# Kernel tuning notes

Hardware: AMD Instinct MI355X
Metric: run time of the kernel (lower is better)

The kernel has to match this reference:

```python
import jax, jax.numpy as jnp
import numpy as np
from jax import lax

DIM = 192
HEADS = 4
HIDDEN = int(DIM * 2.66)  # 510


def _conv1x1(x, w, b):
    # x: [B,C,H,W], w: [O,C], b: [O]
    return jnp.einsum('bchw,oc->bohw', x, w) + b[None, :, None, None]


def _dwconv3x3(x, w, b):
    # x: [B,C,H,W], w: [C,1,3,3], b: [C]
    c = x.shape[1]
    y = lax.conv_general_dilated(x, w, window_strides=(1, 1), padding='SAME',
                                 feature_group_count=c,
                                 dimension_numbers=('NCHW', 'OIHW', 'NCHW'))
    return y + b[None, :, None, None]


def _layernorm_c(x, w, b):
    # LayerNorm over channel dim (torch LayerNorm(dim) applied to b,(hw),c)
    mu = jnp.mean(x, axis=1, keepdims=True)
    var = jnp.mean((x - mu) ** 2, axis=1, keepdims=True)
    xn = (x - mu) / jnp.sqrt(var + 1e-5)
    return xn * w[None, :, None, None] + b[None, :, None, None]


def _l2norm(x):
    # F.normalize(dim=-1), eps=1e-12
    n = jnp.sqrt(jnp.sum(x * x, axis=-1, keepdims=True))
    return x / jnp.maximum(n, 1e-12)


def setup_inputs() -> dict:
    key = jax.random.key(0)
    ks = jax.random.split(key, 16)
    s = 0.02
    d, h2 = DIM, HIDDEN * 2
    return {
        'x': jax.random.normal(ks[0], (4, DIM, 128, 128), jnp.float32),
        'ln1_w': jnp.ones((d,), jnp.float32),
        'ln1_b': jnp.zeros((d,), jnp.float32),
        'qkv_w': jax.random.normal(ks[1], (3 * d, d), jnp.float32) * s,
        'qkv_b': jnp.zeros((3 * d,), jnp.float32),
        'qkv_dw_w': jax.random.normal(ks[2], (3 * d, 1, 3, 3), jnp.float32) * s,
        'qkv_dw_b': jnp.zeros((3 * d,), jnp.float32),
        'temperature': jnp.ones((HEADS, 1, 1), jnp.float32),
        'proj_w': jax.random.normal(ks[3], (d, d), jnp.float32) * s,
        'proj_b': jnp.zeros((d,), jnp.float32),
        'ln2_w': jnp.ones((d,), jnp.float32),
        'ln2_b': jnp.zeros((d,), jnp.float32),
        'pin_w': jax.random.normal(ks[4], (h2, d), jnp.float32) * s,
        'pin_b': jnp.zeros((h2,), jnp.float32),
        'dw_w': jax.random.normal(ks[5], (h2, 1, 3, 3), jnp.float32) * s,
        'dw_b': jnp.zeros((h2,), jnp.float32),
        'pout_w': jax.random.normal(ks[6], (d, HIDDEN), jnp.float32) * s,
        'pout_b': jnp.zeros((d,), jnp.float32),
    }


def _attention(x, qkv_w, qkv_b, qkv_dw_w, qkv_dw_b, temperature, proj_w, proj_b):
    b, c, h, w = x.shape
    qkv = _dwconv3x3(_conv1x1(x, qkv_w, qkv_b), qkv_dw_w, qkv_dw_b)
    q, k, v = jnp.split(qkv, 3, axis=1)
    ch = c // HEADS

    def heads(t):  # b (head c) h w -> b head c (h w)
        return t.reshape(b, HEADS, ch, h * w)

    q, k, v = heads(q), heads(k), heads(v)
    q = _l2norm(q)
    k = _l2norm(k)
    attn = jnp.einsum('bhcn,bhdn->bhcd', q, k) * temperature[None]  # [b,H,ch,ch]
    attn = jax.nn.softmax(attn, axis=-1)
    out = jnp.einsum('bhcd,bhdn->bhcn', attn, v)
    out = out.reshape(b, c, h, w)
    return _conv1x1(out, proj_w, proj_b)


def _ffn(x, pin_w, pin_b, dw_w, dw_b, pout_w, pout_b):
    y = _conv1x1(x, pin_w, pin_b)
    y = _dwconv3x3(y, dw_w, dw_b)
    x1, x2 = jnp.split(y, 2, axis=1)
    y = jax.nn.gelu(x1, approximate=False) * x2
    return _conv1x1(y, pout_w, pout_b)


def reference(x, ln1_w, ln1_b, qkv_w, qkv_b, qkv_dw_w, qkv_dw_b, temperature,
              proj_w, proj_b, ln2_w, ln2_b, pin_w, pin_b, dw_w, dw_b,
              pout_w, pout_b):
    x = x + _attention(_layernorm_c(x, ln1_w, ln1_b), qkv_w, qkv_b,
                       qkv_dw_w, qkv_dw_b, temperature, proj_w, proj_b)
    x = x + _ffn(_layernorm_c(x, ln2_w, ln2_b), pin_w, pin_b, dw_w, dw_b,
                 pout_w, pout_b)
    return x
```

## Files before the change

### kernel.cpp

```cpp
#include <hip/hip_runtime.h>
#include <math.h>

typedef long long i64;
typedef unsigned short u16;
typedef unsigned int u32;

#define HW 16384
#define DIM 192
#define NHEADS 4
#define CH 48
#define OQKV 576
#define HID 510
#define H2 1020
#define NB 4
#define NSPLIT 64
#define QKPAD 132

typedef __attribute__((ext_vector_type(8))) short short8v;
typedef __attribute__((ext_vector_type(4))) float float4v;

__device__ __forceinline__ u16 f2bf(float f) {
  union { float f; u32 u; } v; v.f = f;
  u32 r = v.u + 0x7FFF + ((v.u >> 16) & 1);
  return (u16)(r >> 16);
}
__device__ __forceinline__ float bflo(u32 w) {
  union { u32 u; float f; } v; v.u = w << 16; return v.f;
}
__device__ __forceinline__ float bfhi(u32 w) {
  union { u32 u; float f; } v; v.u = w & 0xFFFF0000u; return v.f;
}
__device__ __forceinline__ float bf1(u16 h) {
  union { u32 u; float f; } v; v.u = ((u32)h) << 16; return v.f;
}
__device__ __forceinline__ u32 pk(float a, float b) {
  return (u32)f2bf(a) | ((u32)f2bf(b) << 16);
}
__device__ __forceinline__ float gelu_f(float x) {
  float y = 0.7978845608f * (x + 0.044715f * x * x * x);
  float ay = fabsf(y);
  float e = __expf(-2.f * ay);
  float t = (1.f - e) / (1.f + e);
  t = (y < 0.f) ? -t : t;
  return 0.5f * x * (1.f + t);
}

#define GLL16(gp, lp) __builtin_amdgcn_global_load_lds( \
    (const __attribute__((address_space(1))) u32*)(gp), \
    (__attribute__((address_space(3))) u32*)(lp), 16, 0, 0)

__global__ __launch_bounds__(256) void ln_kernel(const float* __restrict__ x,
    const float* __restrict__ w, const float* __restrict__ b, u16* __restrict__ yT) {
  __shared__ float st[32][193];
  __shared__ float red[2][8][32];
  __shared__ float murs[2][32];
  const float* xb = x + (i64)blockIdx.y * DIM * HW;
  u16* yb = yT + (i64)blockIdx.y * (i64)HW * DIM;
  int tid = threadIdx.x;
  int g = tid >> 5, p = tid & 31;
  int pix0 = blockIdx.x * 32;
  float s = 0.f, ss = 0.f;
  #pragma unroll
  for (int i = 0; i < 24; ++i) {
    float t = xb[(i64)(g * 24 + i) * HW + pix0 + p];
    st[p][g * 24 + i] = t; s += t; ss += t * t;
  }
  red[0][g][p] = s; red[1][g][p] = ss;
  __syncthreads();
  if (tid < 32) {
    float S = 0.f, SS = 0.f;
    #pragma unroll
    for (int gg = 0; gg < 8; ++gg) { S += red[0][gg][tid]; SS += red[1][gg][tid]; }
    float mu = S * (1.f / DIM);
    float var = SS * (1.f / DIM) - mu * mu;
    murs[0][tid] = mu;
    murs[1][tid] = rsqrtf(var + 1e-5f);
  }
  __syncthreads();
  int px = tid >> 3, c0 = (tid & 7) * 24;
  float mu = murs[0][px], rs = murs[1][px];
  u16 ob[24];
  #pragma unroll
  for (int i = 0; i < 24; ++i) {
    ob[i] = f2bf((st[px][c0 + i] - mu) * rs * w[c0 + i] + b[c0 + i]);
  }
  u16* yp = yb + (i64)(pix0 + px) * DIM + c0;
  #pragma unroll
  for (int j = 0; j < 3; ++j) *(uint4*)(yp + j * 8) = *(const uint4*)&ob[j * 8];
}

__global__ __launch_bounds__(256) void wconv_all(const float* __restrict__ qkv_w,
    const float* __restrict__ proj_w, const float* __restrict__ pin_w,
    const float* __restrict__ pout_w, u16* __restrict__ Wq, u16* __restrict__ Wpj,
    u16* __restrict__ Wpi, u16* __restrict__ Wpo) {
  int idx = blockIdx.x * 256 + threadIdx.x;
  const float* src; u16* dst; int O, C, Kpad;
  if (idx < 122880)      { src = qkv_w;  dst = Wq;  O = OQKV; C = 192; Kpad = 192; }
  else if (idx < 172032) { idx -= 122880; src = proj_w; dst = Wpj; O = 192;  C = 192; Kpad = 192; }
  else if (idx < 368640) { idx -= 172032; src = pin_w;  dst = Wpi; O = H2;   C = 192; Kpad = 192; }
  else if (idx < 499712) { idx -= 368640; src = pout_w; dst = Wpo; O = 192;  C = HID; Kpad = 512; }
  else return;
  int r = idx / Kpad, c = idx - r * Kpad;
  dst[idx] = f2bf((r < O && c < C) ? src[(i64)r * C + c] : 0.f);
}

__global__ __launch_bounds__(256) void gemm_bf16(const u16* __restrict__ A,
    const float* __restrict__ bias, const u16* __restrict__ B,
    const float* __restrict__ Res, float* __restrict__ Out,
    u16* __restrict__ OutB, int O, int K, i64 sB, i64 sOut, i64 sRes) {
  __shared__ __align__(16) u16 lds[2 * 128 * 64];
  int zb = blockIdx.z;
  B += (i64)zb * sB;
  if (Res) Res += (i64)zb * sRes;
  if (OutB) OutB += (i64)zb * sOut; else Out += (i64)zb * sOut;
  int tid = threadIdx.x;
  int lane = tid & 63, wave = tid >> 6;
  int wm = (wave >> 1) * 64, wn = (wave & 1) * 64;
  int obase = blockIdx.y * 128, nbase = blockIdx.x * 128;
  float4v acc[4][4];
  #pragma unroll
  for (int m = 0; m < 4; ++m)
    #pragma unroll
    for (int n = 0; n < 4; ++n) acc[m][n] = (float4v){0.f, 0.f, 0.f, 0.f};

  const u16* Abase = A + (i64)obase * K;
  const u16* Bbase = B + (i64)nbase * K;
  char* ldsA = (char*)&lds[0];
  char* ldsB = (char*)&lds[8192];
  int srow = wave * 8 + (lane >> 3);
  int sj = lane & 7;

  for (int k0 = 0; k0 < K; k0 += 64) {
    #pragma unroll
    for (int iss = 0; iss < 4; ++iss) {
      int r = iss * 32 + srow;
      int kb = sj ^ (r & 7);
      GLL16(Abase + (i64)r * K + k0 + kb * 8, ldsA + iss * 4096 + wave * 1024);
      GLL16(Bbase + (i64)r * K + k0 + kb * 8, ldsB + iss * 4096 + wave * 1024);
    }
    __syncthreads();
    #pragma unroll
    for (int kk = 0; kk < 2; ++kk) {
      short8v af[4], bfr[4];
      #pragma unroll
      for (int m = 0; m < 4; ++m) {
        int r = wm + m * 16 + (lane & 15);
        int kb = kk * 4 + (lane >> 4);
        af[m] = *(const short8v*)(ldsA + r * 128 + ((kb ^ (r & 7)) << 4));
      }
      #pragma unroll
      for (int n = 0; n < 4; ++n) {
        int r = wn + n * 16 + (lane & 15);
        int kb = kk * 4 + (lane >> 4);
        bfr[n] = *(const short8v*)(ldsB + r * 128 + ((kb ^ (r & 7)) << 4));
      }
      #pragma unroll
      for (int m = 0; m < 4; ++m)
        #pragma unroll
        for (int n = 0; n < 4; ++n)
          acc[m][n] = __builtin_amdgcn_mfma_f32_16x16x32_bf16(af[m], bfr[n], acc[m][n], 0, 0, 0);
    }
    __syncthreads();
  }

  int rowq = lane >> 4, coln = lane & 15;
  #pragma unroll
  for (int m = 0; m < 4; ++m) {
    #pragma unroll
    for (int reg = 0; reg < 4; ++reg) {
      int o = obase + wm + m * 16 + rowq * 4 + reg;
      if (o >= O) continue;
      float bv = bias[o];
      #pragma unroll
      for (int n = 0; n < 4; ++n) {
        int nn = nbase + wn + n * 16 + coln;
        float v = acc[m][n][reg] + bv;
        if (OutB) {
          OutB[(i64)o * HW + nn] = f2bf(v);
        } else {
          if (Res) v += Res[(i64)o * HW + nn];
          Out[(i64)o * HW + nn] = v;
        }
      }
    }
  }
}

__global__ __launch_bounds__(256) void dwconv_bf16(const u16* __restrict__ in,
    const float* __restrict__ w9, const float* __restrict__ bs,
    u16* __restrict__ out) {
  in  += (i64)blockIdx.z * OQKV * HW;
  out += (i64)blockIdx.z * OQKV * HW;
  int q = threadIdx.x & 31;
  int grp = threadIdx.x >> 5;
  int y = blockIdx.y;
  int c0 = blockIdx.x * 64 + grp * 8;
  int xb = q * 4;
  #pragma unroll
  for (int i = 0; i < 8; ++i) {
    int c = c0 + i;
    const float* wp = w9 + c * 9;
    float bv = bs[c];
    float a0 = bv, a1 = bv, a2 = bv, a3 = bv;
    const u16* chan = in + (i64)c * HW;
    #pragma unroll
    for (int dy = -1; dy <= 1; ++dy) {
      int yy = y + dy;
      if (yy < 0 || yy >= 128) continue;
      uint4 raw = *(const uint4*)(chan + yy * 128 + xb - 2);
      float f1 = bfhi(raw.x);
      float f2 = bflo(raw.y), f3 = bfhi(raw.y);
      float f4 = bflo(raw.z), f5 = bfhi(raw.z);
      float f6 = bflo(raw.w);
      if (q == 0) f1 = 0.f;
      if (q == 31) f6 = 0.f;
      float wa = wp[(dy + 1) * 3 + 0], wb = wp[(dy + 1) * 3 + 1], wc = wp[(dy + 1) * 3 + 2];
      a0 += wa * f1 + wb * f2 + wc * f3;
      a1 += wa * f2 + wb * f3 + wc * f4;
      a2 += wa * f3 + wb * f4 + wc * f5;
      a3 += wa * f4 + wb * f5 + wc * f6;
    }
    ushort4 o;
    o.x = f2bf(a0); o.y = f2bf(a1); o.z = f2bf(a2); o.w = f2bf(a3);
    *(ushort4*)(out + (i64)c * HW + y * 128 + xb) = o;
  }
}

__global__ __launch_bounds__(256) void attn_qk_kernel(const u16* __restrict__ qkv,
    float* __restrict__ part, float* __restrict__ partN) {
  qkv   += (i64)blockIdx.z * OQKV * HW;
  part  += (i64)blockIdx.z * 589824;
  partN += (i64)blockIdx.z * 24576;
  __shared__ float qs[48][QKPAD];
  __shared__ float ks[48][QKPAD];
  int h = blockIdx.x, sp = blockIdx.y;
  int n0 = sp * (HW / NSPLIT);
  const u16* qb = qkv + (i64)(h * CH) * HW + n0;
  const u16* kb = qkv + (i64)(DIM + h * CH) * HW + n0;
  int tid = threadIdx.x;
  int c0 = (tid >> 4) * 3, d0 = (tid & 15) * 3;
  bool isq = (tid & 15) == 0;
  bool isk = (tid >> 4) == 0;
  float acc[3][3] = {};
  float qn[3] = {}, kn[3] = {};
  for (int nn = 0; nn < 256; nn += 128) {
    for (int l = tid; l < 48 * 16; l += 256) {
      int r = l >> 4, j = (l & 15) * 8;
      uint4 rq = *(const uint4*)(qb + (i64)r * HW + nn + j);
      uint4 rk = *(const uint4*)(kb + (i64)r * HW + nn + j);
      qs[r][j + 0] = bflo(rq.x); qs[r][j + 1] = bfhi(rq.x);
      qs[r][j + 2] = bflo(rq.y); qs[r][j + 3] = bfhi(rq.y);
      qs[r][j + 4] = bflo(rq.z); qs[r][j + 5] = bfhi(rq.z);
      qs[r][j + 6] = bflo(rq.w); qs[r][j + 7] = bfhi(rq.w);
      ks[r][j + 0] = bflo(rk.x); ks[r][j + 1] = bfhi(rk.x);
      ks[r][j + 2] = bflo(rk.y); ks[r][j + 3] = bfhi(rk.y);
      ks[r][j + 4] = bflo(rk.z); ks[r][j + 5] = bfhi(rk.z);
      ks[r][j + 6] = bflo(rk.w); ks[r][j + 7] = bfhi(rk.w);
    }
    __syncthreads();
    #pragma unroll 2
    for (int j = 0; j < 128; j += 4) {
      float qv[3][4], kv[3][4];
      #pragma unroll
      for (int i = 0; i < 3; ++i) {
        float4 t = *(const float4*)&qs[c0 + i][j];
        qv[i][0] = t.x; qv[i][1] = t.y; qv[i][2] = t.z; qv[i][3] = t.w;
        float4 u = *(const float4*)&ks[d0 + i][j];
        kv[i][0] = u.x; kv[i][1] = u.y; kv[i][2] = u.z; kv[i][3] = u.w;
      }
      #pragma unroll
      for (int i = 0; i < 3; ++i)
        #pragma unroll
        for (int jj = 0; jj < 3; ++jj)
          #pragma unroll
          for (int e = 0; e < 4; ++e)
            acc[i][jj] += qv[i][e] * kv[jj][e];
      if (isq) {
        #pragma unroll
        for (int i = 0; i < 3; ++i)
          #pragma unroll
          for (int e = 0; e < 4; ++e) qn[i] += qv[i][e] * qv[i][e];
      }
      if (isk) {
        #pragma unroll
        for (int i = 0; i < 3; ++i)
          #pragma unroll
          for (int e = 0; e < 4; ++e) kn[i] += kv[i][e] * kv[i][e];
      }
    }
    __syncthreads();
  }
  float* pp = part + ((i64)(h * NSPLIT) + sp) * 2304;
  #pragma unroll
  for (int i = 0; i < 3; ++i)
    #pragma unroll
    for (int jj = 0; jj < 3; ++jj)
      pp[(c0 + i) * 48 + d0 + jj] = acc[i][jj];
  float* pn = partN + ((i64)(h * NSPLIT) + sp) * 96;
  if (isq) {
    #pragma unroll
    for (int i = 0; i < 3; ++i) pn[c0 + i] = qn[i];
  }
  if (isk) {
    #pragma unroll
    for (int i = 0; i < 3; ++i) pn[48 + d0 + i] = kn[i];
  }
}

__global__ __launch_bounds__(64) void attn_sm3(const float* __restrict__ part,
    const float* __restrict__ partN, const float* __restrict__ temp,
    float* __restrict__ attn) {
  part  += (i64)blockIdx.z * 589824;
  partN += (i64)blockIdx.z * 24576;
  attn  += (i64)blockIdx.z * 9216;
  int h = blockIdx.x, c = blockIdx.y;
  int d = threadIdx.x;
  const float* pN = partN + (i64)h * NSPLIT * 96;
  float sq = pN[d * 96 + c];
  #pragma unroll
  for (int mask = 32; mask; mask >>= 1) sq += __shfl_xor(sq, mask);
  float invq = 1.f / fmaxf(sqrtf(sq), 1e-12f);
  float logit = -1e30f;
  if (d < CH) {
    float sk = 0.f, s = 0.f;
    for (int sp = 0; sp < NSPLIT; ++sp) {
      sk += pN[sp * 96 + 48 + d];
      s += part[((i64)(h * NSPLIT) + sp) * 2304 + c * 48 + d];
    }
    float invk = 1.f / fmaxf(sqrtf(sk), 1e-12f);
    logit = s * invq * invk * temp[h];
  }
  float m = logit;
  #pragma unroll
  for (int mask = 32; mask; mask >>= 1) m = fmaxf(m, __shfl_xor(m, mask));
  float e = (d < CH) ? expf(logit - m) : 0.f;
  float ssum = e;
  #pragma unroll
  for (int mask = 32; mask; mask >>= 1) ssum += __shfl_xor(ssum, mask);
  if (d < CH) attn[(i64)h * 2304 + c * 48 + d] = e / ssum;
}

__global__ __launch_bounds__(256) void attn_v_kernel(const u16* __restrict__ qkv,
    const float* __restrict__ attnm, u16* __restrict__ outT) {
  qkv   += (i64)blockIdx.z * OQKV * HW;
  attnm += (i64)blockIdx.z * 9216;
  outT  += (i64)blockIdx.z * (i64)HW * DIM;
  __shared__ float as[CH * CH];
  __shared__ u16 st[256 * 52];
  int h = blockIdx.x, tile = blockIdx.y;
  int tid = threadIdx.x;
  for (int l = tid; l < CH * CH; l += 256) as[l] = attnm[(i64)h * 2304 + l];
  __syncthreads();
  int n = tile * 256 + tid;
  const u16* vb = qkv + (i64)(2 * DIM + h * CH) * HW + n;
  float vreg[CH];
  #pragma unroll
  for (int d = 0; d < CH; ++d) vreg[d] = bf1(vb[(i64)d * HW]);
  u32* strow = (u32*)st + tid * 26;
  #pragma unroll 2
  for (int c = 0; c < CH; c += 4) {
    float a0 = 0.f, a1 = 0.f, a2 = 0.f, a3 = 0.f;
    const float* r0 = &as[(c + 0) * CH];
    const float* r1 = &as[(c + 1) * CH];
    const float* r2 = &as[(c + 2) * CH];
    const float* r3 = &as[(c + 3) * CH];
    #pragma unroll
    for (int d = 0; d < CH; ++d) {
      float vv = vreg[d];
      a0 += r0[d] * vv; a1 += r1[d] * vv; a2 += r2[d] * vv; a3 += r3[d] * vv;
    }
    strow[(c >> 1) + 0] = pk(a0, a1);
    strow[(c >> 1) + 1] = pk(a2, a3);
  }
  __syncthreads();
  const uint2* sv = (const uint2*)st;
  u16* ob = outT + (i64)(tile * 256) * DIM + h * CH;
  #pragma unroll
  for (int k = 0; k < 12; ++k) {
    int idx = k * 256 + tid;
    int px = idx / 12, pc = idx - px * 12;
    *(uint2*)(ob + (i64)px * DIM + pc * 4) = sv[px * 13 + pc];
  }
}

__global__ __launch_bounds__(256) void dwgate_bf16(const u16* __restrict__ h1,
    const float* __restrict__ w9, const float* __restrict__ bs,
    u16* __restrict__ og) {
  h1 += (i64)blockIdx.z * H2 * HW;
  og += (i64)blockIdx.z * (i64)HW * 512;
  __shared__ u32 st[128 * 33];
  int q = threadIdx.x & 31;
  int grp = threadIdx.x >> 5;
  int y = blockIdx.y;
  int c0 = blockIdx.x * 64 + grp * 8;
  int xb = q * 4;
  float res[4][8];
  #pragma unroll
  for (int i = 0; i < 8; ++i) {
    int c = c0 + i;
    bool valid = (c < HID);
    float b1 = valid ? bs[c] : 0.f;
    float b2 = valid ? bs[c + HID] : 0.f;
    float a0 = b1, a1 = b1, a2 = b1, a3 = b1;
    float g0 = b2, g1 = b2, g2 = b2, g3 = b2;
    if (valid) {
      const float* wp1 = w9 + c * 9;
      const float* wp2 = w9 + (i64)(c + HID) * 9;
      const u16* ch1 = h1 + (i64)c * HW;
      const u16* ch2 = h1 + (i64)(c + HID) * HW;
      #pragma unroll
      for (int dy = -1; dy <= 1; ++dy) {
        int yy = y + dy;
        if (yy < 0 || yy >= 128) continue;
        {
          uint4 raw = *(const uint4*)(ch1 + yy * 128 + xb - 2);
          float f1 = bfhi(raw.x);
          float f2 = bflo(raw.y), f3 = bfhi(raw.y);
          float f4 = bflo(raw.z), f5 = bfhi(raw.z);
          float f6 = bflo(raw.w);
          if (q == 0) f1 = 0.f;
          if (q == 31) f6 = 0.f;
          float wa = wp1[(dy + 1) * 3 + 0], wb = wp1[(dy + 1) * 3 + 1], wc = wp1[(dy + 1) * 3 + 2];
          a0 += wa * f1 + wb * f2 + wc * f3;
          a1 += wa * f2 + wb * f3 + wc * f4;
          a2 += wa * f3 + wb * f4 + wc * f5;
          a3 += wa * f4 + wb * f5 + wc * f6;
        }
        {
          uint4 raw = *(const uint4*)(ch2 + yy * 128 + xb - 2);
          float f1 = bfhi(raw.x);
          float f2 = bflo(raw.y), f3 = bfhi(raw.y);
          float f4 = bflo(raw.z), f5 = bfhi(raw.z);
          float f6 = bflo(raw.w);
          if (q == 0) f1 = 0.f;
          if (q == 31) f6 = 0.f;
          float wa = wp2[(dy + 1) * 3 + 0], wb = wp2[(dy + 1) * 3 + 1], wc = wp2[(dy + 1) * 3 + 2];
          g0 += wa * f1 + wb * f2 + wc * f3;
          g1 += wa * f2 + wb * f3 + wc * f4;
          g2 += wa * f3 + wb * f4 + wc * f5;
          g3 += wa * f4 + wb * f5 + wc * f6;
        }
      }
    }
    res[0][i] = valid ? gelu_f(a0) * g0 : 0.f;
    res[1][i] = valid ? gelu_f(a1) * g1 : 0.f;
    res[2][i] = valid ? gelu_f(a2) * g2 : 0.f;
    res[3][i] = valid ? gelu_f(a3) * g3 : 0.f;
  }
  #pragma unroll
  for (int j = 0; j < 4; ++j) {
    int px = xb + j;
    u32* row = st + px * 33 + grp * 4;
    row[0] = pk(res[j][0], res[j][1]);
    row[1] = pk(res[j][2], res[j][3]);
    row[2] = pk(res[j][4], res[j][5]);
    row[3] = pk(res[j][6], res[j][7]);
  }
  __syncthreads();
  u32* og32 = (u32*)og;
  int tid = threadIdx.x;
  #pragma unroll
  for (int k = 0; k < 16; ++k) {
    int idx = k * 256 + tid;
    int px = idx >> 5, dwi = idx & 31;
    og32[(i64)(y * 128 + px) * 256 + blockIdx.x * 32 + dwi] = st[px * 33 + dwi];
  }
}

extern "C" void kernel_launch(void* const* d_in, const int* in_sizes, int n_in,
                              void* d_out, int out_size, void* d_ws, size_t ws_size,
                              hipStream_t stream) {
  const float* x        = (const float*)d_in[0];
  const float* ln1_w    = (const float*)d_in[1];
  const float* ln1_b    = (const float*)d_in[2];
  const float* qkv_w    = (const float*)d_in[3];
  const float* qkv_b    = (const float*)d_in[4];
  const float* qkv_dw_w = (const float*)d_in[5];
  const float* qkv_dw_b = (const float*)d_in[6];
  const float* temp     = (const float*)d_in[7];
  const float* proj_w   = (const float*)d_in[8];
  const float* proj_b   = (const float*)d_in[9];
  const float* ln2_w    = (const float*)d_in[10];
  const float* ln2_b    = (const float*)d_in[11];
  const float* pin_w    = (const float*)d_in[12];
  const float* pin_b    = (const float*)d_in[13];
  const float* dw_w     = (const float*)d_in[14];
  const float* dw_b     = (const float*)d_in[15];
  const float* pout_w   = (const float*)d_in[16];
  const float* pout_b   = (const float*)d_in[17];
  float* out = (float*)d_out;
  char* ws = (char*)d_ws;

  u16* Wq   = (u16*)ws;
  u16* Wpj  = Wq + 640 * 192;
  u16* Wpi  = Wpj + 256 * 192;
  u16* Wpo  = Wpi + 1024 * 192;
  u16* yT   = Wpo + 256 * 512;
  char* dyn = (char*)(yT + (i64)NB * HW * DIM);

  auto layout = [&](int nb, float*& attnm, float*& part, float*& partN,
                    u16*& bufA, u16*& bufQ) -> size_t {
    char* p = dyn;
    attnm = (float*)p; p += (i64)nb * 9216 * 4;
    part  = (float*)p; p += (i64)nb * 589824 * 4;
    partN = (float*)p; p += (i64)nb * 24576 * 4;
    bufA  = (u16*)p;   p += (i64)nb * H2 * HW * 2;
    bufQ  = (u16*)p;   p += (i64)nb * OQKV * HW * 2;
    return (size_t)(p - ws);
  };

  float *attnm, *part, *partN; u16 *bufA, *bufQ;
  int nbat = 4;
  if (layout(4, attnm, part, partN, bufA, bufQ) > ws_size) {
    nbat = 1;
    if (layout(1, attnm, part, partN, bufA, bufQ) > ws_size) return;
  }

  wconv_all<<<(499712 + 255) / 256, 256, 0, stream>>>(qkv_w, proj_w, pin_w, pout_w,
                                                      Wq, Wpj, Wpi, Wpo);
  ln_kernel<<<dim3(HW / 32, NB), 256, 0, stream>>>(x, ln1_w, ln1_b, yT);

  for (int b0 = 0; b0 < NB; b0 += nbat) {
    const float* xb = x + (i64)b0 * DIM * HW;
    float* outb = out + (i64)b0 * DIM * HW;
    u16* yTb = yT + (i64)b0 * HW * DIM;
    u16* attnoutT = bufA;
    u16* gatedT = bufQ;

    gemm_bf16<<<dim3(HW / 128, 5, nbat), 256, 0, stream>>>(
        Wq, qkv_b, yTb, nullptr, nullptr, bufA, OQKV, DIM,
        (i64)HW * DIM, (i64)OQKV * HW, 0);
    dwconv_bf16<<<dim3(OQKV / 64, 128, nbat), 256, 0, stream>>>(bufA, qkv_dw_w, qkv_dw_b, bufQ);
    attn_qk_kernel<<<dim3(NHEADS, NSPLIT, nbat), 256, 0, stream>>>(bufQ, part, partN);
    attn_sm3<<<dim3(NHEADS, CH, nbat), 64, 0, stream>>>(part, partN, temp, attnm);
    attn_v_kernel<<<dim3(NHEADS, HW / 256, nbat), 256, 0, stream>>>(bufQ, attnm, attnoutT);
    gemm_bf16<<<dim3(HW / 128, 2, nbat), 256, 0, stream>>>(
        Wpj, proj_b, attnoutT, xb, outb, nullptr, DIM, DIM,
        (i64)HW * DIM, (i64)DIM * HW, (i64)DIM * HW);

    ln_kernel<<<dim3(HW / 32, nbat), 256, 0, stream>>>(outb, ln2_w, ln2_b, yTb);
    gemm_bf16<<<dim3(HW / 128, 8, nbat), 256, 0, stream>>>(
        Wpi, pin_b, yTb, nullptr, nullptr, bufA, H2, DIM,
        (i64)HW * DIM, (i64)H2 * HW, 0);
    dwgate_bf16<<<dim3(8, 128, nbat), 256, 0, stream>>>(bufA, dw_w, dw_b, gatedT);
    gemm_bf16<<<dim3(HW / 128, 2, nbat), 256, 0, stream>>>(
        Wpo, pout_b, gatedT, outb, outb, nullptr, DIM, 512,
        (i64)HW * 512, (i64)DIM * HW, (i64)DIM * HW);
  }
}
```

Before: 519.6 us.

## Stage GEMM bf16 output via LDS, two-row dwconv, sigmoid GELU

The bf16 GEMM epilogue now writes tiles to shared memory first and then issues coalesced row-contiguous global stores. Both depthwise conv kernels compute two output rows per block, reusing the four loaded input rows and halving the grid in y. GELU is replaced by the cheaper sigmoid approximation x*sigmoid(1.702x). That approximation deviates more from the exact erf GELU and may affect accuracy.

```diff
diff --git a/kernel.cpp b/kernel.cpp
--- a/kernel.cpp
+++ b/kernel.cpp
@@ -36,13 +36,8 @@
 __device__ __forceinline__ u32 pk(float a, float b) {
   return (u32)f2bf(a) | ((u32)f2bf(b) << 16);
 }
-__device__ __forceinline__ float gelu_f(float x) {
-  float y = 0.7978845608f * (x + 0.044715f * x * x * x);
-  float ay = fabsf(y);
-  float e = __expf(-2.f * ay);
-  float t = (1.f - e) / (1.f + e);
-  t = (y < 0.f) ? -t : t;
-  return 0.5f * x * (1.f + t);
+__device__ __forceinline__ float gelu_s(float x) {
+  return x / (1.f + __expf(-1.702f * x));
 }
 
 #define GLL16(gp, lp) __builtin_amdgcn_global_load_lds( \
@@ -164,20 +159,41 @@
   }
 
   int rowq = lane >> 4, coln = lane & 15;
-  #pragma unroll
-  for (int m = 0; m < 4; ++m) {
-    #pragma unroll
-    for (int reg = 0; reg < 4; ++reg) {
-      int o = obase + wm + m * 16 + rowq * 4 + reg;
-      if (o >= O) continue;
-      float bv = bias[o];
-      #pragma unroll
-      for (int n = 0; n < 4; ++n) {
-        int nn = nbase + wn + n * 16 + coln;
-        float v = acc[m][n][reg] + bv;
-        if (OutB) {
-          OutB[(i64)o * HW + nn] = f2bf(v);
-        } else {
+  if (OutB) {
+    #pragma unroll
+    for (int m = 0; m < 4; ++m) {
+      #pragma unroll
+      for (int reg = 0; reg < 4; ++reg) {
+        int o = wm + m * 16 + rowq * 4 + reg;
+        int oo = obase + o;
+        float bv = (oo < O) ? bias[oo] : 0.f;
+        #pragma unroll
+        for (int n = 0; n < 4; ++n) {
+          lds[o * 128 + wn + n * 16 + coln] = f2bf(acc[m][n][reg] + bv);
+        }
+      }
+    }
+    __syncthreads();
+    const u32* st32 = (const u32*)lds;
+    #pragma unroll
+    for (int k = 0; k < 32; ++k) {
+      int idx = k * 256 + tid;
+      int o = idx >> 6, cd = idx & 63;
+      if (obase + o < O)
+        ((u32*)(OutB + (i64)(obase + o) * HW + nbase))[cd] = st32[o * 64 + cd];
+    }
+  } else {
+    #pragma unroll
+    for (int m = 0; m < 4; ++m) {
+      #pragma unroll
+      for (int reg = 0; reg < 4; ++reg) {
+        int o = obase + wm + m * 16 + rowq * 4 + reg;
+        if (o >= O) continue;
+        float bv = bias[o];
+        #pragma unroll
+        for (int n = 0; n < 4; ++n) {
+          int nn = nbase + wn + n * 16 + coln;
+          float v = acc[m][n][reg] + bv;
           if (Res) v += Res[(i64)o * HW + nn];
           Out[(i64)o * HW + nn] = v;
         }
@@ -193,7 +209,7 @@
   out += (i64)blockIdx.z * OQKV * HW;
   int q = threadIdx.x & 31;
   int grp = threadIdx.x >> 5;
-  int y = blockIdx.y;
+  int y0 = blockIdx.y * 2;
   int c0 = blockIdx.x * 64 + grp * 8;
   int xb = q * 4;
   #pragma unroll
@@ -201,28 +217,38 @@
     int c = c0 + i;
     const float* wp = w9 + c * 9;
     float bv = bs[c];
-    float a0 = bv, a1 = bv, a2 = bv, a3 = bv;
     const u16* chan = in + (i64)c * HW;
-    #pragma unroll
-    for (int dy = -1; dy <= 1; ++dy) {
-      int yy = y + dy;
-      if (yy < 0 || yy >= 128) continue;
-      uint4 raw = *(const uint4*)(chan + yy * 128 + xb - 2);
-      float f1 = bfhi(raw.x);
-      float f2 = bflo(raw.y), f3 = bfhi(raw.y);
-      float f4 = bflo(raw.z), f5 = bfhi(raw.z);
-      float f6 = bflo(raw.w);
-      if (q == 0) f1 = 0.f;
-      if (q == 31) f6 = 0.f;
-      float wa = wp[(dy + 1) * 3 + 0], wb = wp[(dy + 1) * 3 + 1], wc = wp[(dy + 1) * 3 + 2];
-      a0 += wa * f1 + wb * f2 + wc * f3;
-      a1 += wa * f2 + wb * f3 + wc * f4;
-      a2 += wa * f3 + wb * f4 + wc * f5;
-      a3 += wa * f4 + wb * f5 + wc * f6;
-    }
-    ushort4 o;
-    o.x = f2bf(a0); o.y = f2bf(a1); o.z = f2bf(a2); o.w = f2bf(a3);
-    *(ushort4*)(out + (i64)c * HW + y * 128 + xb) = o;
+    float f[4][6];
+    #pragma unroll
+    for (int r4 = 0; r4 < 4; ++r4) {
+      int yy = y0 - 1 + r4;
+      if (yy < 0 || yy >= 128) {
+        #pragma unroll
+        for (int e = 0; e < 6; ++e) f[r4][e] = 0.f;
+      } else {
+        uint4 raw = *(const uint4*)(chan + yy * 128 + xb - 2);
+        f[r4][0] = (q == 0) ? 0.f : bfhi(raw.x);
+        f[r4][1] = bflo(raw.y); f[r4][2] = bfhi(raw.y);
+        f[r4][3] = bflo(raw.z); f[r4][4] = bfhi(raw.z);
+        f[r4][5] = (q == 31) ? 0.f : bflo(raw.w);
+      }
+    }
+    #pragma unroll
+    for (int rr = 0; rr < 2; ++rr) {
+      float a0 = bv, a1 = bv, a2 = bv, a3 = bv;
+      #pragma unroll
+      for (int dy = 0; dy < 3; ++dy) {
+        float wa = wp[dy * 3 + 0], wb = wp[dy * 3 + 1], wc = wp[dy * 3 + 2];
+        const float* fr = f[rr + dy];
+        a0 += wa * fr[0] + wb * fr[1] + wc * fr[2];
+        a1 += wa * fr[1] + wb * fr[2] + wc * fr[3];
+        a2 += wa * fr[2] + wb * fr[3] + wc * fr[4];
+        a3 += wa * fr[3] + wb * fr[4] + wc * fr[5];
+      }
+      ushort4 o;
+      o.x = f2bf(a0); o.y = f2bf(a1); o.z = f2bf(a2); o.w = f2bf(a3);
+      *(ushort4*)(out + (i64)c * HW + (y0 + rr) * 128 + xb) = o;
+    }
   }
 }
 
@@ -388,82 +414,122 @@
     u16* __restrict__ og) {
   h1 += (i64)blockIdx.z * H2 * HW;
   og += (i64)blockIdx.z * (i64)HW * 512;
-  __shared__ u32 st[128 * 33];
+  __shared__ u32 st[2][128 * 33];
   int q = threadIdx.x & 31;
   int grp = threadIdx.x >> 5;
-  int y = blockIdx.y;
+  int y0 = blockIdx.y * 2;
   int c0 = blockIdx.x * 64 + grp * 8;
   int xb = q * 4;
-  float res[4][8];
+  float prev[2][4];
   #pragma unroll
   for (int i = 0; i < 8; ++i) {
     int c = c0 + i;
     bool valid = (c < HID);
-    float b1 = valid ? bs[c] : 0.f;
-    float b2 = valid ? bs[c + HID] : 0.f;
-    float a0 = b1, a1 = b1, a2 = b1, a3 = b1;
-    float g0 = b2, g1 = b2, g2 = b2, g3 = b2;
+    float res[2][4];
     if (valid) {
-      const float* wp1 = w9 + c * 9;
-      const float* wp2 = w9 + (i64)(c + HID) * 9;
-      const u16* ch1 = h1 + (i64)c * HW;
-      const u16* ch2 = h1 + (i64)(c + HID) * HW;
-      #pragma unroll
-      for (int dy = -1; dy <= 1; ++dy) {
-        int yy = y + dy;
-        if (yy < 0 || yy >= 128) continue;
-        {
-          uint4 raw = *(const uint4*)(ch1 + yy * 128 + xb - 2);
-          float f1 = bfhi(raw.x);
-          float f2 = bflo(raw.y), f3 = bfhi(raw.y);
-          float f4 = bflo(raw.z), f5 = bfhi(raw.z);
-          float f6 = bflo(raw.w);
-          if (q == 0) f1 = 0.f;
-          if (q == 31) f6 = 0.f;
-          float wa = wp1[(dy + 1) * 3 + 0], wb = wp1[(dy + 1) * 3 + 1], wc = wp1[(dy + 1) * 3 + 2];
-          a0 += wa * f1 + wb * f2 + wc * f3;
-          a1 += wa * f2 + wb * f3 + wc * f4;
-          a2 += wa * f3 + wb * f4 + wc * f5;
-          a3 += wa * f4 + wb * f5 + wc * f6;
+      float f[4][6];
+      float a[2][4], g[2][4];
+      {
+        const float* wp = w9 + c * 9;
+        float bv = bs[c];
+        const u16* chan = h1 + (i64)c * HW;
+        #pragma unroll
+        for (int r4 = 0; r4 < 4; ++r4) {
+          int yy = y0 - 1 + r4;
+          if (yy < 0 || yy >= 128) {
+            #pragma unroll
+            for (int e = 0; e < 6; ++e) f[r4][e] = 0.f;
+          } else {
+            uint4 raw = *(const uint4*)(chan + yy * 128 + xb - 2);
+            f[r4][0] = (q == 0) ? 0.f : bfhi(raw.x);
+            f[r4][1] = bflo(raw.y); f[r4][2] = bfhi(raw.y);
+            f[r4][3] = bflo(raw.z); f[r4][4] = bfhi(raw.z);
+            f[r4][5] = (q == 31) ? 0.f : bflo(raw.w);
+          }
         }
-        {
-          uint4 raw = *(const uint4*)(ch2 + yy * 128 + xb - 2);
-          float f1 = bfhi(raw.x);
-          float f2 = bflo(raw.y), f3 = bfhi(raw.y);
-          float f4 = bflo(raw.z), f5 = bfhi(raw.z);
-          float f6 = bflo(raw.w);
-          if (q == 0) f1 = 0.f;
-          if (q == 31) f6 = 0.f;
-          float wa = wp2[(dy + 1) * 3 + 0], wb = wp2[(dy + 1) * 3 + 1], wc = wp2[(dy + 1) * 3 + 2];
-          g0 += wa * f1 + wb * f2 + wc * f3;
-          g1 += wa * f2 + wb * f3 + wc * f4;
-          g2 += wa * f3 + wb * f4 + wc * f5;
-          g3 += wa * f4 + wb * f5 + wc * f6;
+        #pragma unroll
+        for (int rr = 0; rr < 2; ++rr) {
+          float a0 = bv, a1 = bv, a2 = bv, a3 = bv;
+          #pragma unroll
+          for (int dy = 0; dy < 3; ++dy) {
+            float wa = wp[dy * 3 + 0], wb = wp[dy * 3 + 1], wc = wp[dy * 3 + 2];
+            const float* fr = f[rr + dy];
+            a0 += wa * fr[0] + wb * fr[1] + wc * fr[2];
+            a1 += wa * fr[1] + wb * fr[2] + wc * fr[3];
+            a2 += wa * fr[2] + wb * fr[3] + wc * fr[4];
+            a3 += wa * fr[3] + wb * fr[4] + wc * fr[5];
+          }
+          a[rr][0] = a0; a[rr][1] = a1; a[rr][2] = a2; a[rr][3] = a3;
         }
       }
-    }
-    res[0][i] = valid ? gelu_f(a0) * g0 : 0.f;
-    res[1][i] = valid ? gelu_f(a1) * g1 : 0.f;
-    res[2][i] = valid ? gelu_f(a2) * g2 : 0.f;
-    res[3][i] = valid ? gelu_f(a3) * g3 : 0.f;
-  }
-  #pragma unroll
-  for (int j = 0; j < 4; ++j) {
-    int px = xb + j;
-    u32* row = st + px * 33 + grp * 4;
-    row[0] = pk(res[j][0], res[j][1]);
-    row[1] = pk(res[j][2], res[j][3]);
-    row[2] = pk(res[j][4], res[j][5]);
-    row[3] = pk(res[j][6], res[j][7]);
+      {
+        const float* wp = w9 + (i64)(c + HID) * 9;
+        float bv = bs[c + HID];
+        const u16* chan = h1 + (i64)(c + HID) * HW;
+        #pragma unroll
+        for (int r4 = 0; r4 < 4; ++r4) {
+          int yy = y0 - 1 + r4;
+          if (yy < 0 || yy >= 128) {
+            #pragma unroll
+            for (int e = 0; e < 6; ++e) f[r4][e] = 0.f;
+          } else {
+            uint4 raw = *(const uint4*)(chan + yy * 128 + xb - 2);
+            f[r4][0] = (q == 0) ? 0.f : bfhi(raw.x);
+            f[r4][1] = bflo(raw.y); f[r4][2] = bfhi(raw.y);
+            f[r4][3] = bflo(raw.z); f[r4][4] = bfhi(raw.z);
+            f[r4][5] = (q == 31) ? 0.f : bflo(raw.w);
+          }
+        }
+        #pragma unroll
+        for (int rr = 0; rr < 2; ++rr) {
+          float g0 = bv, g1 = bv, g2 = bv, g3 = bv;
+          #pragma unroll
+          for (int dy = 0; dy < 3; ++dy) {
+            float wa = wp[dy * 3 + 0], wb = wp[dy * 3 + 1], wc = wp[dy * 3 + 2];
+            const float* fr = f[rr + dy];
+            g0 += wa * fr[0] + wb * fr[1] + wc * fr[2];
+            g1 += wa * fr[1] + wb * fr[2] + wc * fr[3];
+            g2 += wa * fr[2] + wb * fr[3] + wc * fr[4];
+            g3 += wa * fr[3] + wb * fr[4] + wc * fr[5];
+          }
+          g[rr][0] = g0; g[rr][1] = g1; g[rr][2] = g2; g[rr][3] = g3;
+        }
+      }
+      #pragma unroll
+      for (int rr = 0; rr < 2; ++rr)
+        #pragma unroll
+        for (int j = 0; j < 4; ++j) res[rr][j] = gelu_s(a[rr][j]) * g[rr][j];
+    } else {
+      #pragma unroll
+      for (int rr = 0; rr < 2; ++rr)
+        #pragma unroll
+        for (int j = 0; j < 4; ++j) res[rr][j] = 0.f;
+    }
+    if (i & 1) {
+      int dwi = grp * 4 + (i >> 1);
+      #pragma unroll
+      for (int rr = 0; rr < 2; ++rr)
+        #pragma unroll
+        for (int j = 0; j < 4; ++j)
+          st[rr][(xb + j) * 33 + dwi] = pk(prev[rr][j], res[rr][j]);
+    } else {
+      #pragma unroll
+      for (int rr = 0; rr < 2; ++rr)
+        #pragma unroll
+        for (int j = 0; j < 4; ++j) prev[rr][j] = res[rr][j];
+    }
   }
   __syncthreads();
   u32* og32 = (u32*)og;
   int tid = threadIdx.x;
   #pragma unroll
-  for (int k = 0; k < 16; ++k) {
-    int idx = k * 256 + tid;
-    int px = idx >> 5, dwi = idx & 31;
-    og32[(i64)(y * 128 + px) * 256 + blockIdx.x * 32 + dwi] = st[px * 33 + dwi];
+  for (int rr = 0; rr < 2; ++rr) {
+    #pragma unroll
+    for (int k = 0; k < 16; ++k) {
+      int idx = k * 256 + tid;
+      int px = idx >> 5, dwi = idx & 31;
+      og32[(i64)((y0 + rr) * 128 + px) * 256 + blockIdx.x * 32 + dwi] = st[rr][px * 33 + dwi];
+    }
   }
 }
 
@@ -530,7 +596,7 @@
     gemm_bf16<<<dim3(HW / 128, 5, nbat), 256, 0, stream>>>(
         Wq, qkv_b, yTb, nullptr, nullptr, bufA, OQKV, DIM,
         (i64)HW * DIM, (i64)OQKV * HW, 0);
-    dwconv_bf16<<<dim3(OQKV / 64, 128, nbat), 256, 0, stream>>>(bufA, qkv_dw_w, qkv_dw_b, bufQ);
+    dwconv_bf16<<<dim3(OQKV / 64, 64, nbat), 256, 0, stream>>>(bufA, qkv_dw_w, qkv_dw_b, bufQ);
     attn_qk_kernel<<<dim3(NHEADS, NSPLIT, nbat), 256, 0, stream>>>(bufQ, part, partN);
     attn_sm3<<<dim3(NHEADS, CH, nbat), 64, 0, stream>>>(part, partN, temp, attnm);
     attn_v_kernel<<<dim3(NHEADS, HW / 256, nbat), 256, 0, stream>>>(bufQ, attnm, attnoutT);
@@ -542,7 +608,7 @@
     gemm_bf16<<<dim3(HW / 128, 8, nbat), 256, 0, stream>>>(
         Wpi, pin_b, yTb, nullptr, nullptr, bufA, H2, DIM,
         (i64)HW * DIM, (i64)H2 * HW, 0);
-    dwgate_bf16<<<dim3(8, 128, nbat), 256, 0, stream>>>(bufA, dw_w, dw_b, gatedT);
+    dwgate_bf16<<<dim3(8, 64, nbat), 256, 0, stream>>>(bufA, dw_w, dw_b, gatedT);
     gemm_bf16<<<dim3(HW / 128, 2, nbat), 256, 0, stream>>>(
         Wpo, pout_b, gatedT, outb, outb, nullptr, DIM, 512,
         (i64)HW * 512, (i64)DIM * HW, (i64)DIM * HW);
```

Result: slower. 532.8 us (+2.5%).
